# Performance work log

Measured on AMD Instinct MI355X. Metric: run time of the kernel, lower is better.

Reference implementation:

```python
import jax, jax.numpy as jnp
import numpy as np

B, L, C = 128, 512, 128


def setup_inputs() -> dict:
    key = jax.random.key(0)
    k1, k2, k3, k4, k5 = jax.random.split(key, 5)
    emissions = jax.random.normal(k1, (B, L, C), dtype=jnp.float32)
    tags = jax.random.randint(k2, (B, L), 0, C, dtype=jnp.int64)
    mask = jnp.ones((B, L), dtype=bool)
    transitions = jax.random.uniform(k3, (C, C), minval=-0.1, maxval=0.1, dtype=jnp.float32)
    start_transitions = jax.random.uniform(k4, (C,), minval=-0.1, maxval=0.1, dtype=jnp.float32)
    end_transitions = jax.random.uniform(k5, (C,), minval=-0.1, maxval=0.1, dtype=jnp.float32)
    return {
        "emissions": emissions,
        "tags": tags,
        "mask": mask,
        "transitions": transitions,
        "start_transitions": start_transitions,
        "end_transitions": end_transitions,
    }


def _sequence_score(emissions, tags, mask, transitions, start_transitions, end_transitions):
    # emissions: [B,L,C], tags/mask: [B,L]
    b, l = tags.shape
    score = start_transitions[tags[:, 0]]
    score = score + jnp.take_along_axis(emissions[:, 0], tags[:, 0:1], axis=1)[:, 0]
    # vectorized over t=1..L-1
    trans = transitions[tags[:, :-1], tags[:, 1:]]                                  # [B,L-1]
    emit = jnp.take_along_axis(emissions[:, 1:], tags[:, 1:, None], axis=2)[..., 0]  # [B,L-1]
    active = mask[:, 1:].astype(emissions.dtype)
    score = score + jnp.sum((trans + emit) * active, axis=1)
    last_idx = jnp.sum(mask.astype(jnp.int32), axis=1) - 1                           # [B]
    last_tags = jnp.take_along_axis(tags, last_idx[:, None], axis=1)[:, 0]
    score = score + end_transitions[last_tags]
    return score


def _partition(emissions, mask, transitions, start_transitions, end_transitions):
    alpha0 = start_transitions[None, :] + emissions[:, 0]  # [B,C]

    def step(alpha, xs):
        emit_t, mask_t = xs  # [B,C], [B]
        # logsumexp over previous tag: alpha[b,i] + transitions[i,j]
        nxt = jax.nn.logsumexp(alpha[:, :, None] + transitions[None, :, :], axis=1) + emit_t
        alpha = jnp.where(mask_t[:, None], nxt, alpha)
        return alpha, None

    xs = (jnp.swapaxes(emissions[:, 1:], 0, 1), jnp.swapaxes(mask[:, 1:], 0, 1))  # [L-1,B,C],[L-1,B]
    alpha, _ = jax.lax.scan(step, alpha0, xs)
    return jax.nn.logsumexp(alpha + end_transitions[None, :], axis=1)  # [B]


def reference(emissions, tags, mask, transitions, start_transitions, end_transitions):
    safe_tags = jnp.where(tags == -100, 0, tags)
    score = _sequence_score(emissions, safe_tags, mask, transitions, start_transitions, end_transitions)
    partition = _partition(emissions, mask, transitions, start_transitions, end_transitions)
    ll = score - partition
    return -jnp.mean(ll)
```

## Files before the change

### kernel.cpp

```cpp
#include <hip/hip_runtime.h>


typedef _Float16 half2_t __attribute__((ext_vector_type(2)));

#define L2E 1.4426950408889634f
#define LN2 0.6931471805599453f

__device__ __forceinline__ float fexp2(float x) { return __builtin_amdgcn_exp2f(x); }
__device__ __forceinline__ float flog2(float x) { return __builtin_amdgcn_logf(x); }

__device__ __forceinline__ float rfl(float x) {
    return __builtin_bit_cast(float, __builtin_amdgcn_readfirstlane(__builtin_bit_cast(int, x)));
}
__device__ __forceinline__ int expo_of(float x) {
    return (int)((__builtin_bit_cast(unsigned int, x) >> 23) & 255u) - 127;
}
__device__ __forceinline__ float dot2(half2_t a, half2_t b, float c) {
#if __has_builtin(__builtin_amdgcn_fdot2)
    return __builtin_amdgcn_fdot2(a, b, c, false);
#else
    return fmaf((float)a.x, (float)b.x, fmaf((float)a.y, (float)b.y, c));
#endif
}
__device__ __forceinline__ half2_t pk16(float a, float b) {
#if __has_builtin(__builtin_amdgcn_cvt_pkrtz)
    return __builtin_bit_cast(half2_t, __builtin_amdgcn_cvt_pkrtz(a, b));
#else
    half2_t r; r.x = (_Float16)a; r.y = (_Float16)b; return r;
#endif
}

__global__ void zero_out_kernel(float* o) {
    if (threadIdx.x == 0 && blockIdx.x == 0) o[0] = 0.0f;
}

#define STEP(EV, CUR, NXT) do {                                              \
    const float e0b = rfl(EV.x);                                             \
    const int   df  = expo_of(rfl(Pshadow)) + 8 + (int)(L2E * e0b);          \
    const float dff = (float)df;                                             \
    const float4* __restrict__ p4 = (const float4*)&pbuf[CUR][0];            \
    float s00=0.f,s01=0.f,s02=0.f,s03=0.f;                                   \
    float s10=0.f,s11=0.f,s12=0.f,s13=0.f;                                   \
    _Pragma("unroll")                                                        \
    for (int k = 0; k < 16; ++k) {                                           \
        const float4 v = p4[k];                                              \
        const half2_t h0 = __builtin_bit_cast(half2_t, v.x);                 \
        const half2_t h1 = __builtin_bit_cast(half2_t, v.y);                 \
        const half2_t h2 = __builtin_bit_cast(half2_t, v.z);                 \
        const half2_t h3 = __builtin_bit_cast(half2_t, v.w);                 \
        s00 = dot2(h0, Ee[4*k+0], s00);  s10 = dot2(h0, Eo[4*k+0], s10);     \
        s01 = dot2(h1, Ee[4*k+1], s01);  s11 = dot2(h1, Eo[4*k+1], s11);     \
        s02 = dot2(h2, Ee[4*k+2], s02);  s12 = dot2(h2, Eo[4*k+2], s12);     \
        s03 = dot2(h3, Ee[4*k+3], s03);  s13 = dot2(h3, Eo[4*k+3], s13);     \
    }                                                                        \
    const float me = fexp2(fmaf(L2E, EV.x, -dff));                           \
    const float mo = fexp2(fmaf(L2E, EV.y, -dff));                           \
    float Pe = (((s00+s01)+(s02+s03))) * me;                                 \
    float Po = (((s10+s11)+(s12+s13))) * mo;                                 \
    Pe = fminf(Pe, 60000.0f);  Po = fminf(Po, 60000.0f);                     \
    pbuf[NXT][l] = __builtin_bit_cast(int, pk16(Pe, Po));                    \
    Pshadow = Pe;                                                            \
    c += df;                                                                 \
} while (0)

__launch_bounds__(64, 1)
__global__ void crf_fwd_kernel(const float* __restrict__ emis,
                               const int*   __restrict__ tags,
                               const float* __restrict__ trans,
                               const float* __restrict__ startT,
                               const float* __restrict__ endT,
                               float* __restrict__ out)
{
    constexpr int L = 512;
    constexpr int C = 128;
    const int b  = blockIdx.x;
    const int l  = threadIdx.x;
    const int j0 = 2 * l;
    const int j1 = 2 * l + 1;

    __shared__ __align__(16) int pbuf[2][64];

    const float*  eb = emis + (size_t)b * L * C;
    const int*    tb = tags + (size_t)b * L;
    const float2* e2 = (const float2*)eb;
    const float2* t2 = (const float2*)trans;

    half2_t Ee[64], Eo[64];
    #pragma unroll
    for (int m = 0; m < 64; ++m) {
        const float2 r0 = t2[(2*m)     * 64 + l];
        const float2 r1 = t2[(2*m + 1) * 64 + l];
        Ee[m] = pk16(__expf(r0.x), __expf(r1.x));
        Eo[m] = pk16(__expf(r0.y), __expf(r1.y));
    }

    float sp = 0.0f;
    #pragma unroll
    for (int k = 0; k < 8; ++k) {
        const int t  = l + 64 * k;
        const int tg = tb[t];
        float cb = eb[t * C + tg];
        if (t == 0)     cb += startT[tg];
        else            cb += trans[tb[t - 1] * C + tg];
        if (t == L - 1) cb += endT[tg];
        sp += cb;
    }

    const float a2e = L2E * (startT[j0] + eb[j0]);
    const float a2o = L2E * (startT[j1] + eb[j1]);
    const int   d0  = (int)rfl(a2e);
    const float P0i = fexp2(a2e - (float)d0);
    const float P1i = fexp2(a2o - (float)d0);
    int   c = d0;
    float Pshadow = P0i;
    pbuf[0][l] = __builtin_bit_cast(int, pk16(P0i, P1i));

    float2 eA = e2[1 * 64 + l];
    float2 eB = e2[2 * 64 + l];

    for (int k = 0; k < 255; ++k) {
        STEP(eA, 0, 1);
        eA = e2[(2*k + 3) * 64 + l];
        STEP(eB, 1, 0);
        int t3 = 2*k + 4; if (t3 > L - 1) t3 = L - 1;
        eB = e2[t3 * 64 + l];
    }
    STEP(eA, 0, 1);

    const half2_t ph = __builtin_bit_cast(half2_t, pbuf[1][l]);
    float q = (float)ph.x * fexp2(L2E * endT[j0])
            + (float)ph.y * fexp2(L2E * endT[j1]);

    #pragma unroll
    for (int off = 32; off > 0; off >>= 1) {
        q  += __shfl_down(q,  off);
        sp += __shfl_down(sp, off);
    }
    if (l == 0) {
        const float part = ((float)c + flog2(q)) * LN2;
        atomicAdd(out, (part - sp) * (1.0f / 128.0f));
    }
}

extern "C" void kernel_launch(void* const* d_in, const int* in_sizes, int n_in,
                              void* d_out, int out_size, void* d_ws, size_t ws_size,
                              hipStream_t stream) {
    const float* emis   = (const float*)d_in[0];
    const int*   tags   = (const int*)  d_in[1];
    const float* trans  = (const float*)d_in[3];
    const float* startT = (const float*)d_in[4];
    const float* endT   = (const float*)d_in[5];
    float* out = (float*)d_out;

    zero_out_kernel<<<1, 64, 0, stream>>>(out);
    crf_fwd_kernel<<<128, 64, 0, stream>>>(emis, tags, trans, startT, endT, out);
}
```

Before: 272.6 us.

## Broadcast alpha vector via readlane into SGPRs instead of LDS double buffer

Replaces the shared-memory ping-pong buffer that carried the packed fp16 alpha vector between recurrence steps with 64 v_readlane broadcasts into a scalar register array. The goal is to take the LDS write-then-read round trip off the serial 511-step critical path. The shift exponent now comes from the fp16 bits of lane 0's value instead of a float shadow copy. The catch is 64 serial readlane instructions per step, heavy SGPR pressure, and possible spills or extra latency. The final q also uses the unrounded fp32 Pe/Po instead of the fp16 copies.

```diff
diff --git a/kernel.cpp b/kernel.cpp
--- a/kernel.cpp
+++ b/kernel.cpp
@@ -12,54 +12,45 @@
 __device__ __forceinline__ float rfl(float x) {
     return __builtin_bit_cast(float, __builtin_amdgcn_readfirstlane(__builtin_bit_cast(int, x)));
 }
-__device__ __forceinline__ int expo_of(float x) {
-    return (int)((__builtin_bit_cast(unsigned int, x) >> 23) & 255u) - 127;
-}
 __device__ __forceinline__ float dot2(half2_t a, half2_t b, float c) {
-#if __has_builtin(__builtin_amdgcn_fdot2)
     return __builtin_amdgcn_fdot2(a, b, c, false);
-#else
-    return fmaf((float)a.x, (float)b.x, fmaf((float)a.y, (float)b.y, c));
-#endif
 }
 __device__ __forceinline__ half2_t pk16(float a, float b) {
-#if __has_builtin(__builtin_amdgcn_cvt_pkrtz)
     return __builtin_bit_cast(half2_t, __builtin_amdgcn_cvt_pkrtz(a, b));
-#else
-    half2_t r; r.x = (_Float16)a; r.y = (_Float16)b; return r;
-#endif
 }
 
 __global__ void zero_out_kernel(float* o) {
     if (threadIdx.x == 0 && blockIdx.x == 0) o[0] = 0.0f;
 }
 
-#define STEP(EV, CUR, NXT) do {                                              \
+#define STEP(EV) do {                                                        \
+    const unsigned p0b = (unsigned)sp[0];                                    \
+    const int ex = (int)((p0b >> 10) & 31u) - 15;                            \
     const float e0b = rfl(EV.x);                                             \
-    const int   df  = expo_of(rfl(Pshadow)) + 8 + (int)(L2E * e0b);          \
+    const int df = ex + 8 + (int)(L2E * e0b);                                \
     const float dff = (float)df;                                             \
-    const float4* __restrict__ p4 = (const float4*)&pbuf[CUR][0];            \
+    const float me = fexp2(fmaf(L2E, EV.x, -dff));                           \
+    const float mo = fexp2(fmaf(L2E, EV.y, -dff));                           \
     float s00=0.f,s01=0.f,s02=0.f,s03=0.f;                                   \
     float s10=0.f,s11=0.f,s12=0.f,s13=0.f;                                   \
     _Pragma("unroll")                                                        \
-    for (int k = 0; k < 16; ++k) {                                           \
-        const float4 v = p4[k];                                              \
-        const half2_t h0 = __builtin_bit_cast(half2_t, v.x);                 \
-        const half2_t h1 = __builtin_bit_cast(half2_t, v.y);                 \
-        const half2_t h2 = __builtin_bit_cast(half2_t, v.z);                 \
-        const half2_t h3 = __builtin_bit_cast(half2_t, v.w);                 \
-        s00 = dot2(h0, Ee[4*k+0], s00);  s10 = dot2(h0, Eo[4*k+0], s10);     \
-        s01 = dot2(h1, Ee[4*k+1], s01);  s11 = dot2(h1, Eo[4*k+1], s11);     \
-        s02 = dot2(h2, Ee[4*k+2], s02);  s12 = dot2(h2, Eo[4*k+2], s12);     \
-        s03 = dot2(h3, Ee[4*k+3], s03);  s13 = dot2(h3, Eo[4*k+3], s13);     \
+    for (int i = 0; i < 16; ++i) {                                           \
+        const half2_t h0 = __builtin_bit_cast(half2_t, sp[4*i+0]);           \
+        const half2_t h1 = __builtin_bit_cast(half2_t, sp[4*i+1]);           \
+        const half2_t h2 = __builtin_bit_cast(half2_t, sp[4*i+2]);           \
+        const half2_t h3 = __builtin_bit_cast(half2_t, sp[4*i+3]);           \
+        s00 = dot2(h0, Ee[4*i+0], s00);  s10 = dot2(h0, Eo[4*i+0], s10);     \
+        s01 = dot2(h1, Ee[4*i+1], s01);  s11 = dot2(h1, Eo[4*i+1], s11);     \
+        s02 = dot2(h2, Ee[4*i+2], s02);  s12 = dot2(h2, Eo[4*i+2], s12);     \
+        s03 = dot2(h3, Ee[4*i+3], s03);  s13 = dot2(h3, Eo[4*i+3], s13);     \
     }                                                                        \
-    const float me = fexp2(fmaf(L2E, EV.x, -dff));                           \
-    const float mo = fexp2(fmaf(L2E, EV.y, -dff));                           \
-    float Pe = (((s00+s01)+(s02+s03))) * me;                                 \
-    float Po = (((s10+s11)+(s12+s13))) * mo;                                 \
+    Pe = (((s00+s01)+(s02+s03))) * me;                                       \
+    Po = (((s10+s11)+(s12+s13))) * mo;                                       \
     Pe = fminf(Pe, 60000.0f);  Po = fminf(Po, 60000.0f);                     \
-    pbuf[NXT][l] = __builtin_bit_cast(int, pk16(Pe, Po));                    \
-    Pshadow = Pe;                                                            \
+    const int pknew = __builtin_bit_cast(int, pk16(Pe, Po));                 \
+    _Pragma("unroll")                                                        \
+    for (int i = 0; i < 64; ++i)                                             \
+        sp[i] = __builtin_amdgcn_readlane(pknew, i);                         \
     c += df;                                                                 \
 } while (0)
 
@@ -78,8 +69,6 @@
     const int j0 = 2 * l;
     const int j1 = 2 * l + 1;
 
-    __shared__ __align__(16) int pbuf[2][64];
-
     const float*  eb = emis + (size_t)b * L * C;
     const int*    tb = tags + (size_t)b * L;
     const float2* e2 = (const float2*)eb;
@@ -94,7 +83,7 @@
         Eo[m] = pk16(__expf(r0.y), __expf(r1.y));
     }
 
-    float sp = 0.0f;
+    float sp_score = 0.0f;
     #pragma unroll
     for (int k = 0; k < 8; ++k) {
         const int t  = l + 64 * k;
@@ -103,42 +92,47 @@
         if (t == 0)     cb += startT[tg];
         else            cb += trans[tb[t - 1] * C + tg];
         if (t == L - 1) cb += endT[tg];
-        sp += cb;
+        sp_score += cb;
     }
 
     const float a2e = L2E * (startT[j0] + eb[j0]);
     const float a2o = L2E * (startT[j1] + eb[j1]);
     const int   d0  = (int)rfl(a2e);
-    const float P0i = fexp2(a2e - (float)d0);
-    const float P1i = fexp2(a2o - (float)d0);
+    float Pe = fexp2(a2e - (float)d0);
+    float Po = fexp2(a2o - (float)d0);
     int   c = d0;
-    float Pshadow = P0i;
-    pbuf[0][l] = __builtin_bit_cast(int, pk16(P0i, P1i));
+
+    int sp[64];
+    {
+        const int pk0 = __builtin_bit_cast(int, pk16(Pe, Po));
+        #pragma unroll
+        for (int i = 0; i < 64; ++i)
+            sp[i] = __builtin_amdgcn_readlane(pk0, i);
+    }
 
     float2 eA = e2[1 * 64 + l];
     float2 eB = e2[2 * 64 + l];
 
     for (int k = 0; k < 255; ++k) {
-        STEP(eA, 0, 1);
+        STEP(eA);
         eA = e2[(2*k + 3) * 64 + l];
-        STEP(eB, 1, 0);
+        STEP(eB);
         int t3 = 2*k + 4; if (t3 > L - 1) t3 = L - 1;
         eB = e2[t3 * 64 + l];
     }
-    STEP(eA, 0, 1);
+    STEP(eA);
 
-    const half2_t ph = __builtin_bit_cast(half2_t, pbuf[1][l]);
-    float q = (float)ph.x * fexp2(L2E * endT[j0])
-            + (float)ph.y * fexp2(L2E * endT[j1]);
+    float q = Pe * fexp2(L2E * endT[j0])
+            + Po * fexp2(L2E * endT[j1]);
 
     #pragma unroll
     for (int off = 32; off > 0; off >>= 1) {
-        q  += __shfl_down(q,  off);
-        sp += __shfl_down(sp, off);
+        q        += __shfl_down(q,        off);
+        sp_score += __shfl_down(sp_score, off);
     }
     if (l == 0) {
         const float part = ((float)c + flog2(q)) * LN2;
-        atomicAdd(out, (part - sp) * (1.0f / 128.0f));
+        atomicAdd(out, (part - sp_score) * (1.0f / 128.0f));
     }
 }
 
```

After: 295.1 us. +8.2%, slower.
